# Kernel tuning notes

Measured on AMD Instinct MI355X. Metric: run time of the kernel, lower is better.

The kernel has to match this reference:

```python
import jax, jax.numpy as jnp
import numpy as np

HEAD_SIZE = 64
B, T, C = 8, 2048, 768
NEG_FILL = -99999999999999.0  # exact constant from the source


def setup_inputs() -> dict:
    key = jax.random.key(0)
    kx, kk, kq, kv = jax.random.split(key, 4)
    x = jax.random.normal(kx, (B, T, C), dtype=jnp.float32)
    # Dense(head_size, use_bias=False) kernels, glorot-ish scale
    s = 1.0 / np.sqrt(C)
    Wk = jax.random.normal(kk, (C, HEAD_SIZE), dtype=jnp.float32) * s
    Wq = jax.random.normal(kq, (C, HEAD_SIZE), dtype=jnp.float32) * s
    Wv = jax.random.normal(kv, (C, HEAD_SIZE), dtype=jnp.float32) * s
    return {"x": x, "Wk": Wk, "Wq": Wq, "Wv": Wv}


def reference(x, Wk, Wq, Wv):
    # x: [B, T, C]
    k = jnp.einsum("btc,cd->btd", x, Wk)  # [B, T, D]
    q = jnp.einsum("btc,cd->btd", x, Wq)
    v = jnp.einsum("btc,cd->btd", x, Wv)
    raw_affinity = jnp.einsum("btd,bsd->bts", q, k)  # [B, T, T]
    t = x.shape[1]
    tri = jnp.tril(jnp.ones((t, t), dtype=jnp.float32))
    # faithful to source: multiplicative mask, scale applied AFTER masking
    mask_mult = jnp.where(tri == 1.0, 1.0, NEG_FILL)
    logits = raw_affinity * mask_mult * (HEAD_SIZE ** -0.5)
    attn = jax.nn.softmax(logits, axis=-1)
    out = jnp.einsum("bts,bsd->btd", attn, v)  # [B, T, D]
    return out
```

## Files before the change

kernel.cpp:

```cpp
#include <hip/hip_runtime.h>
#include <math.h>

#define BATCH 8
#define SEQ   2048
#define CDIM  768
#define HDIM  64
#define QROWS 32
#define NBLK  (SEQ / 64)

typedef float f4 __attribute__((ext_vector_type(4)));
typedef short s8 __attribute__((ext_vector_type(8)));

static __device__ __forceinline__ int swz_off(int dp, int grp) {
    return ((dp + grp) & 31) * 2;
}
static __device__ __forceinline__ unsigned bf16_rne(float f) {
    unsigned u = __float_as_uint(f);
    return (u + 0x7FFFu + ((u >> 16) & 1u)) >> 16;
}

__global__ __launch_bounds__(256) void qkv_proj_kernel(
    const float* __restrict__ x,
    const float* __restrict__ Wk,
    const float* __restrict__ Wq,
    const float* __restrict__ Wv,
    double* __restrict__ qd,
    double* __restrict__ kd,
    float*  __restrict__ vf)
{
    __shared__ float xs[32][68];
    __shared__ float wqs[64 * 64];
    __shared__ float wks[64 * 64];
    __shared__ float wvs[64 * 64];

    const int tid = threadIdx.x;
    const int tx  = tid & 15;
    const int ty  = tid >> 4;
    const size_t row0 = (size_t)blockIdx.x * 32;

    double qa[2][4] = {{0, 0, 0, 0}, {0, 0, 0, 0}};
    double ka[2][4] = {{0, 0, 0, 0}, {0, 0, 0, 0}};
    float  va[2][4] = {{0, 0, 0, 0}, {0, 0, 0, 0}};

    for (int cc = 0; cc < CDIM; cc += 64) {
        __syncthreads();
        #pragma unroll
        for (int it = 0; it < 2; ++it) {
            const int t  = tid + it * 256;
            const int r  = t >> 4;
            const int c4 = t & 15;
            const float4 v4 = *reinterpret_cast<const float4*>(
                &x[(row0 + r) * CDIM + cc + c4 * 4]);
            *reinterpret_cast<float4*>(&xs[r][c4 * 4]) = v4;
        }
        {
            const float4* wqg = reinterpret_cast<const float4*>(&Wq[(size_t)cc * HDIM]);
            const float4* wkg = reinterpret_cast<const float4*>(&Wk[(size_t)cc * HDIM]);
            const float4* wvg = reinterpret_cast<const float4*>(&Wv[(size_t)cc * HDIM]);
            float4* wql = reinterpret_cast<float4*>(wqs);
            float4* wkl = reinterpret_cast<float4*>(wks);
            float4* wvl = reinterpret_cast<float4*>(wvs);
            #pragma unroll
            for (int it = 0; it < 4; ++it) {
                const int t = tid + it * 256;
                wql[t] = wqg[t];
                wkl[t] = wkg[t];
                wvl[t] = wvg[t];
            }
        }
        __syncthreads();
        #pragma unroll 4
        for (int c = 0; c < 64; ++c) {
            const float4 wq4 = *reinterpret_cast<const float4*>(&wqs[c * 64 + tx * 4]);
            const float4 wk4 = *reinterpret_cast<const float4*>(&wks[c * 64 + tx * 4]);
            const float4 wv4 = *reinterpret_cast<const float4*>(&wvs[c * 64 + tx * 4]);
            #pragma unroll
            for (int i = 0; i < 2; ++i) {
                const float  xv = xs[ty * 2 + i][c];
                const double xd = (double)xv;
                qa[i][0] += xd * (double)wq4.x;
                qa[i][1] += xd * (double)wq4.y;
                qa[i][2] += xd * (double)wq4.z;
                qa[i][3] += xd * (double)wq4.w;
                ka[i][0] += xd * (double)wk4.x;
                ka[i][1] += xd * (double)wk4.y;
                ka[i][2] += xd * (double)wk4.z;
                ka[i][3] += xd * (double)wk4.w;
                va[i][0] += xv * wv4.x;
                va[i][1] += xv * wv4.y;
                va[i][2] += xv * wv4.z;
                va[i][3] += xv * wv4.w;
            }
        }
    }
    #pragma unroll
    for (int i = 0; i < 2; ++i) {
        const size_t row = row0 + ty * 2 + i;
        *reinterpret_cast<double2*>(&qd[row * HDIM + tx * 4])     = make_double2(qa[i][0], qa[i][1]);
        *reinterpret_cast<double2*>(&qd[row * HDIM + tx * 4 + 2]) = make_double2(qa[i][2], qa[i][3]);
        *reinterpret_cast<double2*>(&kd[row * HDIM + tx * 4])     = make_double2(ka[i][0], ka[i][1]);
        *reinterpret_cast<double2*>(&kd[row * HDIM + tx * 4 + 2]) = make_double2(ka[i][2], ka[i][3]);
        *reinterpret_cast<float4*>(&vf[row * HDIM + tx * 4]) =
            make_float4(va[i][0], va[i][1], va[i][2], va[i][3]);
    }
}

__global__ __launch_bounds__(256, 2) void attn_kernel(
    const double* __restrict__ qd,
    const double* __restrict__ kd,
    const float*  __restrict__ vf,
    float* __restrict__ out)
{
    __shared__ __align__(16) double qs[QROWS * 64];
    __shared__ __align__(16) double ks[64 * 64];
    __shared__ __align__(16) float  vs[64 * 66];
    __shared__ __align__(16) unsigned short ps[QROWS * 64];
    __shared__ float sf_row[QROWS];
    __shared__ float l_row[QROWS];

    const int tid  = threadIdx.x;
    const int lane = tid & 63;
    const int w    = tid >> 6;
    const int lo   = lane & 15;
    const int hi   = lane >> 4;
    const int tx   = tid & 15;
    const int ty   = tid >> 4;
    const int tb   = blockIdx.x;
    const int b    = blockIdx.y;
    const int r0   = tb * QROWS;

    const int c2 = tid & 31;
    const int rb = tid >> 5;

    {
        const double* qsrc = qd + ((size_t)b * SEQ + r0) * HDIM;
        #pragma unroll
        for (int it = 0; it < 4; ++it) {
            const int r = rb + it * 8;
            const double2 v2 = *reinterpret_cast<const double2*>(
                &qsrc[(size_t)r * HDIM + 2 * c2]);
            *reinterpret_cast<double2*>(&qs[r * 64 + swz_off(c2, r >> 2)]) = v2;
        }
    }

    double m[2];
    float  l[2];
    f4     acc[2];
    m[0] = m[1] = -1.0e300;
    l[0] = l[1] = 0.f;
    acc[0] = (f4){0.f, 0.f, 0.f, 0.f};
    acc[1] = (f4){0.f, 0.f, 0.f, 0.f};

    double2 kreg[8];
    float4  vreg[4];
    {
        const size_t kvbase = (size_t)b * SEQ * HDIM;
        #pragma unroll
        for (int it = 0; it < 8; ++it)
            kreg[it] = *reinterpret_cast<const double2*>(
                &kd[kvbase + (size_t)(rb + it * 8) * HDIM + 2 * c2]);
        #pragma unroll
        for (int it = 0; it < 4; ++it) {
            const int t = tid + it * 256;
            vreg[it] = *reinterpret_cast<const float4*>(
                &vf[kvbase + (size_t)(t >> 4) * HDIM + (t & 15) * 4]);
        }
    }
    #pragma unroll
    for (int it = 0; it < 8; ++it) {
        const int r = rb + it * 8;
        *reinterpret_cast<double2*>(&ks[r * 64 + swz_off(c2, r >> 2)]) = kreg[it];
    }
    #pragma unroll
    for (int it = 0; it < 4; ++it) {
        const int t = tid + it * 256;
        const int s = t >> 4, c4 = t & 15;
        const int base = s * 66 + 4 * c4;
        *reinterpret_cast<float2*>(&vs[base])     = make_float2(vreg[it].x, vreg[it].y);
        *reinterpret_cast<float2*>(&vs[base + 2]) = make_float2(vreg[it].z, vreg[it].w);
    }
    __syncthreads();

    const int qg = ty >> 1;
    const int mt = w & 1;
    const int nh = w >> 1;

    for (int sb = 0; sb < NBLK; ++sb) {
        if (sb + 1 < NBLK) {
            const size_t kvbase = ((size_t)b * SEQ + (size_t)(sb + 1) * 64) * HDIM;
            #pragma unroll
            for (int it = 0; it < 8; ++it)
                kreg[it] = *reinterpret_cast<const double2*>(
                    &kd[kvbase + (size_t)(rb + it * 8) * HDIM + 2 * c2]);
            #pragma unroll
            for (int it = 0; it < 4; ++it) {
                const int t = tid + it * 256;
                vreg[it] = *reinterpret_cast<const float4*>(
                    &vf[kvbase + (size_t)(t >> 4) * HDIM + (t & 15) * 4]);
            }
        }

        double s[2][4];
        #pragma unroll
        for (int i = 0; i < 2; ++i)
            #pragma unroll
            for (int j = 0; j < 4; ++j) s[i][j] = 0.0;

        #pragma unroll 4
        for (int dp = 0; dp < 32; ++dp) {
            const int qo = swz_off(dp, qg);
            const int ko = swz_off(dp, tx);
            const double2 q0 = *reinterpret_cast<const double2*>(&qs[(2 * ty)     * 64 + qo]);
            const double2 q1 = *reinterpret_cast<const double2*>(&qs[(2 * ty + 1) * 64 + qo]);
            #pragma unroll
            for (int j = 0; j < 4; ++j) {
                const double2 kv = *reinterpret_cast<const double2*>(&ks[(4 * tx + j) * 64 + ko]);
                s[0][j] += q0.x * kv.x + q0.y * kv.y;
                s[1][j] += q1.x * kv.x + q1.y * kv.y;
            }
        }

        #pragma unroll
        for (int i = 0; i < 2; ++i) {
            const int rloc = 2 * ty + i;
            const int rg   = r0 + rloc;
            double lg[4];
            double tm = -1.0e300;
            #pragma unroll
            for (int j = 0; j < 4; ++j) {
                const int cg = sb * 64 + 4 * tx + j;
                const double raw = s[i][j];
                const double logit = (cg <= rg)
                    ? (raw * 1.0) * 0.125
                    : (raw * -99999999999999.0) * 0.125;
                lg[j] = logit;
                tm = fmax(tm, logit);
            }
            #pragma unroll
            for (int off = 8; off > 0; off >>= 1)
                tm = fmax(tm, __shfl_xor(tm, off, 16));
            const double mnew = fmax(m[i], tm);
            const double dm   = m[i] - mnew;
            const float  sf   = (dm < -80.0) ? 0.f : expf((float)dm);
            m[i] = mnew;
            l[i] *= sf;
            float p[4];
            float psum = 0.f;
            #pragma unroll
            for (int j = 0; j < 4; ++j) {
                const double dlt = lg[j] - mnew;
                p[j] = (dlt < -80.0) ? 0.f : expf((float)dlt);
                psum += p[j];
            }
            {
                const unsigned xr = (unsigned)((rloc & 7) << 4);
                char* base = reinterpret_cast<char*>(ps) + rloc * 128;
                const unsigned w0 = bf16_rne(p[0]) | (bf16_rne(p[1]) << 16);
                const unsigned w1 = bf16_rne(p[2]) | (bf16_rne(p[3]) << 16);
                *reinterpret_cast<unsigned*>(base + (((unsigned)(8 * tx))     ^ xr)) = w0;
                *reinterpret_cast<unsigned*>(base + (((unsigned)(8 * tx + 4)) ^ xr)) = w1;
            }
            #pragma unroll
            for (int off = 8; off > 0; off >>= 1)
                psum += __shfl_xor(psum, off, 16);
            l[i] += psum;
            if (tx == 0) sf_row[rloc] = sf;
        }
        __syncthreads();

        #pragma unroll
        for (int i = 0; i < 4; ++i) {
            const float sfr = sf_row[16 * mt + 4 * hi + i];
            acc[0][i] *= sfr;
            acc[1][i] *= sfr;
        }
        #pragma unroll
        for (int ks_ = 0; ks_ < 2; ++ks_) {
            const int arow  = 16 * mt + lo;
            const unsigned abyte = (unsigned)(arow * 128)
                + (((unsigned)(64 * ks_ + 16 * hi)) ^ ((unsigned)((arow & 7) << 4)));
            const s8 af = *reinterpret_cast<const s8*>(
                reinterpret_cast<const char*>(ps) + abyte);
            const int kb = 32 * ks_ + 8 * hi;
            #pragma unroll
            for (int ntl = 0; ntl < 2; ++ntl) {
                const int dcol = 16 * (2 * nh + ntl) + lo;
                union { unsigned u[4]; s8 v; } bu;
                #pragma unroll
                for (int e2 = 0; e2 < 4; ++e2) {
                    const float f0 = vs[(kb + 2 * e2)     * 66 + dcol];
                    const float f1 = vs[(kb + 2 * e2 + 1) * 66 + dcol];
                    bu.u[e2] = bf16_rne(f0) | (bf16_rne(f1) << 16);
                }
                acc[ntl] = __builtin_amdgcn_mfma_f32_16x16x32_bf16(af, bu.v, acc[ntl], 0, 0, 0);
            }
        }
        __syncthreads();

        if (sb + 1 < NBLK) {
            #pragma unroll
            for (int it = 0; it < 8; ++it) {
                const int r = rb + it * 8;
                *reinterpret_cast<double2*>(&ks[r * 64 + swz_off(c2, r >> 2)]) = kreg[it];
            }
            #pragma unroll
            for (int it = 0; it < 4; ++it) {
                const int t = tid + it * 256;
                const int s_ = t >> 4, c4 = t & 15;
                const int base = s_ * 66 + 4 * c4;
                *reinterpret_cast<float2*>(&vs[base])     = make_float2(vreg[it].x, vreg[it].y);
                *reinterpret_cast<float2*>(&vs[base + 2]) = make_float2(vreg[it].z, vreg[it].w);
            }
            __syncthreads();
        }
    }

    if (tx == 0) {
        l_row[2 * ty]     = l[0];
        l_row[2 * ty + 1] = l[1];
    }
    __syncthreads();

    #pragma unroll
    for (int ntl = 0; ntl < 2; ++ntl) {
        const int d = 16 * (2 * nh + ntl) + lo;
        #pragma unroll
        for (int i = 0; i < 4; ++i) {
            const int row = 16 * mt + 4 * hi + i;
            out[((size_t)b * SEQ + r0 + row) * HDIM + d] = acc[ntl][i] / l_row[row];
        }
    }
}

extern "C" void kernel_launch(void* const* d_in, const int* in_sizes, int n_in,
                              void* d_out, int out_size, void* d_ws, size_t ws_size,
                              hipStream_t stream)
{
    const float* x  = (const float*)d_in[0];
    const float* Wk = (const float*)d_in[1];
    const float* Wq = (const float*)d_in[2];
    const float* Wv = (const float*)d_in[3];
    float* out = (float*)d_out;

    double* qd = (double*)d_ws;
    double* kd = qd + (size_t)BATCH * SEQ * HDIM;
    float*  vf = (float*)(kd + (size_t)BATCH * SEQ * HDIM);

    qkv_proj_kernel<<<dim3(512), dim3(256), 0, stream>>>(x, Wk, Wq, Wv, qd, kd, vf);
    attn_kernel<<<dim3(SEQ / QROWS, BATCH), dim3(256), 0, stream>>>(qd, kd, vf, out);
}
```

Baseline: 396.8 us.

## Store V transposed in bf16 and halve KV tile to 32 rows

The projection kernel now writes V as transposed bf16 (per batch, D x T), so the attention kernel can load MFMA B operands directly from LDS as 8-element vectors. This replaces the per-element fp32 reads and bf16 conversions done inside the inner loop. The KV tile shrinks from 64 to 32 rows, which halves LDS use, allows raising launch bounds to 4 blocks per SM, and cuts per-thread score registers. The cost is twice as many loop iterations and barriers, and scattered 2-byte transposed stores in the projection kernel.

```diff
diff --git a/kernel.cpp b/kernel.cpp
--- a/kernel.cpp
+++ b/kernel.cpp
@@ -6,7 +6,8 @@
 #define CDIM  768
 #define HDIM  64
 #define QROWS 32
-#define NBLK  (SEQ / 64)
+#define KVB   32
+#define NIT   (SEQ / KVB)
 
 typedef float f4 __attribute__((ext_vector_type(4)));
 typedef short s8 __attribute__((ext_vector_type(8)));
@@ -18,6 +19,8 @@
     unsigned u = __float_as_uint(f);
     return (u + 0x7FFFu + ((u >> 16) & 1u)) >> 16;
 }
+
+#define MASKC (-99999999999999.0 * 0.125)
 
 __global__ __launch_bounds__(256) void qkv_proj_kernel(
     const float* __restrict__ x,
@@ -26,7 +29,7 @@
     const float* __restrict__ Wv,
     double* __restrict__ qd,
     double* __restrict__ kd,
-    float*  __restrict__ vf)
+    unsigned short* __restrict__ vtg)
 {
     __shared__ float xs[32][68];
     __shared__ float wqs[64 * 64];
@@ -100,21 +103,25 @@
         *reinterpret_cast<double2*>(&qd[row * HDIM + tx * 4 + 2]) = make_double2(qa[i][2], qa[i][3]);
         *reinterpret_cast<double2*>(&kd[row * HDIM + tx * 4])     = make_double2(ka[i][0], ka[i][1]);
         *reinterpret_cast<double2*>(&kd[row * HDIM + tx * 4 + 2]) = make_double2(ka[i][2], ka[i][3]);
-        *reinterpret_cast<float4*>(&vf[row * HDIM + tx * 4]) =
-            make_float4(va[i][0], va[i][1], va[i][2], va[i][3]);
-    }
-}
-
-__global__ __launch_bounds__(256, 2) void attn_kernel(
+        const int brow = (int)(row >> 11);
+        const int trow = (int)(row & (SEQ - 1));
+        #pragma unroll
+        for (int j = 0; j < 4; ++j)
+            vtg[(size_t)brow * (HDIM * SEQ) + (size_t)(4 * tx + j) * SEQ + trow] =
+                (unsigned short)bf16_rne(va[i][j]);
+    }
+}
+
+__global__ __launch_bounds__(256, 4) void attn_kernel(
     const double* __restrict__ qd,
     const double* __restrict__ kd,
-    const float*  __restrict__ vf,
+    const unsigned short* __restrict__ vtg,
     float* __restrict__ out)
 {
     __shared__ __align__(16) double qs[QROWS * 64];
-    __shared__ __align__(16) double ks[64 * 64];
-    __shared__ __align__(16) float  vs[64 * 66];
-    __shared__ __align__(16) unsigned short ps[QROWS * 64];
+    __shared__ __align__(16) double ks[KVB * 64];
+    __shared__ __align__(16) unsigned short vT[64 * 40];
+    __shared__ __align__(16) unsigned short ps[QROWS * 40];
     __shared__ float sf_row[QROWS];
     __shared__ float l_row[QROWS];
 
@@ -131,6 +138,8 @@
 
     const int c2 = tid & 31;
     const int rb = tid >> 5;
+    const int vd = tid >> 2;
+    const int vch = tid & 3;
 
     {
         const double* qsrc = qd + ((size_t)b * SEQ + r0) * HDIM;
@@ -151,91 +160,66 @@
     acc[0] = (f4){0.f, 0.f, 0.f, 0.f};
     acc[1] = (f4){0.f, 0.f, 0.f, 0.f};
 
-    double2 kreg[8];
-    float4  vreg[4];
+    double2 kreg[4];
+    uint4   vreg;
     {
         const size_t kvbase = (size_t)b * SEQ * HDIM;
         #pragma unroll
-        for (int it = 0; it < 8; ++it)
+        for (int it = 0; it < 4; ++it)
             kreg[it] = *reinterpret_cast<const double2*>(
                 &kd[kvbase + (size_t)(rb + it * 8) * HDIM + 2 * c2]);
-        #pragma unroll
-        for (int it = 0; it < 4; ++it) {
-            const int t = tid + it * 256;
-            vreg[it] = *reinterpret_cast<const float4*>(
-                &vf[kvbase + (size_t)(t >> 4) * HDIM + (t & 15) * 4]);
-        }
+        vreg = *reinterpret_cast<const uint4*>(
+            &vtg[(size_t)b * (HDIM * SEQ) + (size_t)vd * SEQ + 8 * vch]);
     }
     #pragma unroll
-    for (int it = 0; it < 8; ++it) {
+    for (int it = 0; it < 4; ++it) {
         const int r = rb + it * 8;
         *reinterpret_cast<double2*>(&ks[r * 64 + swz_off(c2, r >> 2)]) = kreg[it];
     }
-    #pragma unroll
-    for (int it = 0; it < 4; ++it) {
-        const int t = tid + it * 256;
-        const int s = t >> 4, c4 = t & 15;
-        const int base = s * 66 + 4 * c4;
-        *reinterpret_cast<float2*>(&vs[base])     = make_float2(vreg[it].x, vreg[it].y);
-        *reinterpret_cast<float2*>(&vs[base + 2]) = make_float2(vreg[it].z, vreg[it].w);
-    }
+    *reinterpret_cast<uint4*>(&vT[vd * 40 + 8 * vch]) = vreg;
     __syncthreads();
 
     const int qg = ty >> 1;
     const int mt = w & 1;
     const int nh = w >> 1;
 
-    for (int sb = 0; sb < NBLK; ++sb) {
-        if (sb + 1 < NBLK) {
-            const size_t kvbase = ((size_t)b * SEQ + (size_t)(sb + 1) * 64) * HDIM;
-            #pragma unroll
-            for (int it = 0; it < 8; ++it)
+    for (int sb = 0; sb < NIT; ++sb) {
+        if (sb + 1 < NIT) {
+            const size_t kvbase = ((size_t)b * SEQ + (size_t)(sb + 1) * KVB) * HDIM;
+            #pragma unroll
+            for (int it = 0; it < 4; ++it)
                 kreg[it] = *reinterpret_cast<const double2*>(
                     &kd[kvbase + (size_t)(rb + it * 8) * HDIM + 2 * c2]);
-            #pragma unroll
-            for (int it = 0; it < 4; ++it) {
-                const int t = tid + it * 256;
-                vreg[it] = *reinterpret_cast<const float4*>(
-                    &vf[kvbase + (size_t)(t >> 4) * HDIM + (t & 15) * 4]);
-            }
-        }
-
-        double s[2][4];
-        #pragma unroll
-        for (int i = 0; i < 2; ++i)
-            #pragma unroll
-            for (int j = 0; j < 4; ++j) s[i][j] = 0.0;
-
+            vreg = *reinterpret_cast<const uint4*>(
+                &vtg[(size_t)b * (HDIM * SEQ) + (size_t)vd * SEQ
+                     + (size_t)(sb + 1) * KVB + 8 * vch]);
+        }
+
+        double s00 = 0.0, s01 = 0.0, s10 = 0.0, s11 = 0.0;
         #pragma unroll 4
         for (int dp = 0; dp < 32; ++dp) {
             const int qo = swz_off(dp, qg);
-            const int ko = swz_off(dp, tx);
+            const int ko = swz_off(dp, tx >> 1);
             const double2 q0 = *reinterpret_cast<const double2*>(&qs[(2 * ty)     * 64 + qo]);
             const double2 q1 = *reinterpret_cast<const double2*>(&qs[(2 * ty + 1) * 64 + qo]);
-            #pragma unroll
-            for (int j = 0; j < 4; ++j) {
-                const double2 kv = *reinterpret_cast<const double2*>(&ks[(4 * tx + j) * 64 + ko]);
-                s[0][j] += q0.x * kv.x + q0.y * kv.y;
-                s[1][j] += q1.x * kv.x + q1.y * kv.y;
-            }
-        }
-
+            const double2 k0 = *reinterpret_cast<const double2*>(&ks[(2 * tx)     * 64 + ko]);
+            const double2 k1 = *reinterpret_cast<const double2*>(&ks[(2 * tx + 1) * 64 + ko]);
+            s00 += q0.x * k0.x + q0.y * k0.y;
+            s01 += q0.x * k1.x + q0.y * k1.y;
+            s10 += q1.x * k0.x + q1.y * k0.y;
+            s11 += q1.x * k1.x + q1.y * k1.y;
+        }
+
+        const int c0 = sb * KVB + 2 * tx;
         #pragma unroll
         for (int i = 0; i < 2; ++i) {
             const int rloc = 2 * ty + i;
             const int rg   = r0 + rloc;
-            double lg[4];
-            double tm = -1.0e300;
-            #pragma unroll
-            for (int j = 0; j < 4; ++j) {
-                const int cg = sb * 64 + 4 * tx + j;
-                const double raw = s[i][j];
-                const double logit = (cg <= rg)
-                    ? (raw * 1.0) * 0.125
-                    : (raw * -99999999999999.0) * 0.125;
-                lg[j] = logit;
-                tm = fmax(tm, logit);
-            }
+            const double raw0 = i ? s10 : s00;
+            const double raw1 = i ? s11 : s01;
+            const double lg0 = raw0 * ((c0     <= rg) ? 0.125 : MASKC);
+            const double lg1 = raw1 * ((c0 + 1 <= rg) ? 0.125 : MASKC);
+            double tm = fmax(lg0, lg1);
             #pragma unroll
             for (int off = 8; off > 0; off >>= 1)
                 tm = fmax(tm, __shfl_xor(tm, off, 16));
@@ -244,22 +228,12 @@
             const float  sf   = (dm < -80.0) ? 0.f : expf((float)dm);
             m[i] = mnew;
             l[i] *= sf;
-            float p[4];
-            float psum = 0.f;
-            #pragma unroll
-            for (int j = 0; j < 4; ++j) {
-                const double dlt = lg[j] - mnew;
-                p[j] = (dlt < -80.0) ? 0.f : expf((float)dlt);
-                psum += p[j];
-            }
-            {
-                const unsigned xr = (unsigned)((rloc & 7) << 4);
-                char* base = reinterpret_cast<char*>(ps) + rloc * 128;
-                const unsigned w0 = bf16_rne(p[0]) | (bf16_rne(p[1]) << 16);
-                const unsigned w1 = bf16_rne(p[2]) | (bf16_rne(p[3]) << 16);
-                *reinterpret_cast<unsigned*>(base + (((unsigned)(8 * tx))     ^ xr)) = w0;
-                *reinterpret_cast<unsigned*>(base + (((unsigned)(8 * tx + 4)) ^ xr)) = w1;
-            }
+            const double d0 = lg0 - mnew, d1 = lg1 - mnew;
+            const float p0 = (d0 < -80.0) ? 0.f : expf((float)d0);
+            const float p1 = (d1 < -80.0) ? 0.f : expf((float)d1);
+            *reinterpret_cast<unsigned*>(&ps[rloc * 40 + 2 * tx]) =
+                bf16_rne(p0) | (bf16_rne(p1) << 16);
+            float psum = p0 + p1;
             #pragma unroll
             for (int off = 8; off > 0; off >>= 1)
                 psum += __shfl_xor(psum, off, 16);
@@ -274,43 +248,24 @@
             acc[0][i] *= sfr;
             acc[1][i] *= sfr;
         }
-        #pragma unroll
-        for (int ks_ = 0; ks_ < 2; ++ks_) {
-            const int arow  = 16 * mt + lo;
-            const unsigned abyte = (unsigned)(arow * 128)
-                + (((unsigned)(64 * ks_ + 16 * hi)) ^ ((unsigned)((arow & 7) << 4)));
-            const s8 af = *reinterpret_cast<const s8*>(
-                reinterpret_cast<const char*>(ps) + abyte);
-            const int kb = 32 * ks_ + 8 * hi;
+        {
+            const s8 af = *reinterpret_cast<const s8*>(&ps[(16 * mt + lo) * 40 + 8 * hi]);
             #pragma unroll
             for (int ntl = 0; ntl < 2; ++ntl) {
-                const int dcol = 16 * (2 * nh + ntl) + lo;
-                union { unsigned u[4]; s8 v; } bu;
-                #pragma unroll
-                for (int e2 = 0; e2 < 4; ++e2) {
-                    const float f0 = vs[(kb + 2 * e2)     * 66 + dcol];
-                    const float f1 = vs[(kb + 2 * e2 + 1) * 66 + dcol];
-                    bu.u[e2] = bf16_rne(f0) | (bf16_rne(f1) << 16);
-                }
-                acc[ntl] = __builtin_amdgcn_mfma_f32_16x16x32_bf16(af, bu.v, acc[ntl], 0, 0, 0);
+                const int d = 16 * (2 * nh + ntl) + lo;
+                const s8 bf = *reinterpret_cast<const s8*>(&vT[d * 40 + 8 * hi]);
+                acc[ntl] = __builtin_amdgcn_mfma_f32_16x16x32_bf16(af, bf, acc[ntl], 0, 0, 0);
             }
         }
         __syncthreads();
 
-        if (sb + 1 < NBLK) {
-            #pragma unroll
-            for (int it = 0; it < 8; ++it) {
+        if (sb + 1 < NIT) {
+            #pragma unroll
+            for (int it = 0; it < 4; ++it) {
                 const int r = rb + it * 8;
                 *reinterpret_cast<double2*>(&ks[r * 64 + swz_off(c2, r >> 2)]) = kreg[it];
             }
-            #pragma unroll
-            for (int it = 0; it < 4; ++it) {
-                const int t = tid + it * 256;
-                const int s_ = t >> 4, c4 = t & 15;
-                const int base = s_ * 66 + 4 * c4;
-                *reinterpret_cast<float2*>(&vs[base])     = make_float2(vreg[it].x, vreg[it].y);
-                *reinterpret_cast<float2*>(&vs[base + 2]) = make_float2(vreg[it].z, vreg[it].w);
-            }
+            *reinterpret_cast<uint4*>(&vT[vd * 40 + 8 * vch]) = vreg;
             __syncthreads();
         }
     }
@@ -344,8 +299,8 @@
 
     double* qd = (double*)d_ws;
     double* kd = qd + (size_t)BATCH * SEQ * HDIM;
-    float*  vf = (float*)(kd + (size_t)BATCH * SEQ * HDIM);
-
-    qkv_proj_kernel<<<dim3(512), dim3(256), 0, stream>>>(x, Wk, Wq, Wv, qd, kd, vf);
-    attn_kernel<<<dim3(SEQ / QROWS, BATCH), dim3(256), 0, stream>>>(qd, kd, vf, out);
-}
+    unsigned short* vtg = (unsigned short*)(kd + (size_t)BATCH * SEQ * HDIM);
+
+    qkv_proj_kernel<<<dim3(512), dim3(256), 0, stream>>>(x, Wk, Wq, Wv, qd, kd, vtg);
+    attn_kernel<<<dim3(SEQ / QROWS, BATCH), dim3(256), 0, stream>>>(qd, kd, vtg, out);
+}
```

Result: slower. 491.8 us (+23.9%).
